# Kernel optimization log

Measured on AMD Instinct MI355X. Metric: run time of the kernel, lower is better.

The kernel has to match this reference:

```python
import jax, jax.numpy as jnp
import numpy as np

H = 1024   # hidden_size
L = 2      # num_layers
T = 32     # num_tracks
B = 512    # batch


def setup_inputs() -> dict:
    key = jax.random.key(0)
    ks = jax.random.split(key, 8)
    s = 1.0 / np.sqrt(H)  # PyTorch LSTM/Linear init scale
    z = jax.random.normal(ks[0], (B, H), jnp.float32)
    W_ih = jax.random.uniform(ks[1], (L, 4 * H, H), jnp.float32, -s, s)
    W_hh = jax.random.uniform(ks[2], (L, 4 * H, H), jnp.float32, -s, s)
    b_ih = jax.random.uniform(ks[3], (L, 4 * H), jnp.float32, -s, s)
    b_hh = jax.random.uniform(ks[4], (L, 4 * H), jnp.float32, -s, s)
    to_h_W = jax.random.uniform(ks[5], (L * H, H), jnp.float32, -s, s)
    to_h_b = jax.random.uniform(ks[6], (L * H,), jnp.float32, -s, s)
    init_emb = jax.random.normal(ks[7], (1, H), jnp.float32)  # nn.Embedding(1, H)
    return {"z": z, "to_h_W": to_h_W, "to_h_b": to_h_b, "init_emb": init_emb,
            "W_ih": W_ih, "W_hh": W_hh, "b_ih": b_ih, "b_hh": b_hh}


def reference(z, to_h_W, to_h_b, init_emb, W_ih, W_hh, b_ih, b_hh):
    bsz = z.shape[0]
    # h init from z: [B, L*H] -> [L, B, H]; c init zeros
    h0 = jnp.tanh(z @ to_h_W.T + to_h_b).reshape(bsz, L, H).transpose(1, 0, 2)
    c0 = jnp.zeros_like(h0)
    # initial input token embedding (index 0 for all batch entries)
    x0 = jnp.broadcast_to(init_emb[0], (bsz, H))

    def step(carry, _):
        x, h, c = carry
        hs, cs = [], []
        for l in range(L):  # fixed small layer loop
            # PyTorch gate order: i, f, g, o
            gates = x @ W_ih[l].T + b_ih[l] + h[l] @ W_hh[l].T + b_hh[l]
            i_g, f_g, g_g, o_g = jnp.split(gates, 4, axis=-1)
            c_new = jax.nn.sigmoid(f_g) * c[l] + jax.nn.sigmoid(i_g) * jnp.tanh(g_g)
            h_new = jax.nn.sigmoid(o_g) * jnp.tanh(c_new)
            hs.append(h_new)
            cs.append(c_new)
            x = h_new  # output of layer l is input of layer l+1
        return (x, jnp.stack(hs), jnp.stack(cs)), x

    _, ys = jax.lax.scan(step, (x0, h0, c0), None, length=T)
    return ys  # [T, B, H] == stacked list of per-track embeddings
```

## Files before the change

### kernel.cpp

```cpp
#include <hip/hip_runtime.h>
#include <cstdint>

typedef __attribute__((ext_vector_type(8))) short short8;
typedef __attribute__((ext_vector_type(4))) float f32x4;
typedef unsigned short u16;

#define HD 1024
#define BSZ 512
#define NL 2
#define TSTEPS 32
#define BM 64
#define BN 128
#define BK 64

__device__ __forceinline__ u16 f2bf(float x) {
  union { float f; uint32_t u; } v; v.f = x;
  uint32_t r = v.u + 0x7FFFu + ((v.u >> 16) & 1u);
  return (u16)(r >> 16);
}
__device__ __forceinline__ float sigm(float x) { return 1.f / (1.f + __expf(-x)); }
__device__ __forceinline__ float tanhfast(float x) { return 1.f - 2.f / (__expf(2.f * x) + 1.f); }

__global__ void pack_w2(const float* __restrict__ Wih, const float* __restrict__ Whh,
                        u16* __restrict__ W2) {
  int idx = blockIdx.x * 256 + threadIdx.x;
  int l   = idx >> 20;
  int rem = idx & 0xFFFFF;
  int np  = rem >> 8;
  int k   = (rem & 255) << 3;
  int gate = (np >> 4) & 3;
  int j    = ((np >> 6) << 4) | (np & 15);
  int n    = (gate << 10) | j;
  const float* src = (k < HD) ? (Wih + ((size_t)(l * 4096 + n) << 10) + k)
                              : (Whh + ((size_t)(l * 4096 + n) << 10) + (k - HD));
  float4 a = reinterpret_cast<const float4*>(src)[0];
  float4 b = reinterpret_cast<const float4*>(src)[1];
  union { u16 s[8]; short8 v; } o;
  o.s[0]=f2bf(a.x); o.s[1]=f2bf(a.y); o.s[2]=f2bf(a.z); o.s[3]=f2bf(a.w);
  o.s[4]=f2bf(b.x); o.s[5]=f2bf(b.y); o.s[6]=f2bf(b.z); o.s[7]=f2bf(b.w);
  *reinterpret_cast<short8*>(W2 + (((size_t)l * 4096 + np) << 11) + k) = o.v;
}

__global__ void pack_thw(const float* __restrict__ thw, u16* __restrict__ dst) {
  int idx = blockIdx.x * 256 + threadIdx.x;
  size_t off = (size_t)idx << 3;
  float4 a = reinterpret_cast<const float4*>(thw + off)[0];
  float4 b = reinterpret_cast<const float4*>(thw + off)[1];
  union { u16 s[8]; short8 v; } o;
  o.s[0]=f2bf(a.x); o.s[1]=f2bf(a.y); o.s[2]=f2bf(a.z); o.s[3]=f2bf(a.w);
  o.s[4]=f2bf(b.x); o.s[5]=f2bf(b.y); o.s[6]=f2bf(b.z); o.s[7]=f2bf(b.w);
  *reinterpret_cast<short8*>(dst + off) = o.v;
}

__global__ void pack_small(const float* __restrict__ z, const float* __restrict__ emb,
                           const float* __restrict__ bih, const float* __restrict__ bhh,
                           u16* __restrict__ zb, u16* __restrict__ xb,
                           float* __restrict__ bias2) {
  int idx = blockIdx.x * 256 + threadIdx.x;
  if (idx < 65536) {
    size_t off = (size_t)idx << 3;
    float4 a = reinterpret_cast<const float4*>(z + off)[0];
    float4 b = reinterpret_cast<const float4*>(z + off)[1];
    union { u16 s[8]; short8 v; } o;
    o.s[0]=f2bf(a.x); o.s[1]=f2bf(a.y); o.s[2]=f2bf(a.z); o.s[3]=f2bf(a.w);
    o.s[4]=f2bf(b.x); o.s[5]=f2bf(b.y); o.s[6]=f2bf(b.z); o.s[7]=f2bf(b.w);
    *reinterpret_cast<short8*>(zb + off) = o.v;
  } else if (idx < 131072) {
    size_t off = (size_t)(idx - 65536) << 3;
    int k = (int)(off & 1023);
    float4 a = reinterpret_cast<const float4*>(emb + k)[0];
    float4 b = reinterpret_cast<const float4*>(emb + k)[1];
    union { u16 s[8]; short8 v; } o;
    o.s[0]=f2bf(a.x); o.s[1]=f2bf(a.y); o.s[2]=f2bf(a.z); o.s[3]=f2bf(a.w);
    o.s[4]=f2bf(b.x); o.s[5]=f2bf(b.y); o.s[6]=f2bf(b.z); o.s[7]=f2bf(b.w);
    *reinterpret_cast<short8*>(xb + off) = o.v;
  } else if (idx < 139264) {
    int q = idx - 131072;
    int l = q >> 12, np = q & 4095;
    int gate = (np >> 4) & 3;
    int j    = ((np >> 6) << 4) | (np & 15);
    int n    = (gate << 10) | j;
    bias2[(l << 12) + np] = bih[(l << 12) + n] + bhh[(l << 12) + n];
  }
}

template<int EPI>
__global__ __launch_bounds__(256, 1)
void lstm_gemm(const u16* __restrict__ A0, const u16* __restrict__ A1,
               const u16* __restrict__ W, const float* __restrict__ bias,
               float* __restrict__ cb0, float* __restrict__ cb1,
               u16* __restrict__ hb0, u16* __restrict__ hb1,
               float* __restrict__ yout, int K)
{
  __shared__ u16 smem[3 * 12288];
  const int tid  = threadIdx.x;
  const int lane = tid & 63;
  const int wave = tid >> 6;
  const int wr = wave >> 1, wc = wave & 1;
  const int lr = lane & 15, lk = lane >> 4;

  int bx, by;
  if constexpr (EPI == 0) {
    bx = blockIdx.x & 15; by = blockIdx.x >> 4;
  } else {
    int xcd = blockIdx.x & 7, win = blockIdx.x >> 3;
    bx = xcd * 4 + (win >> 3);
    by = win & 7;
  }
  const int m0 = by * BM;
  const int n0 = bx * BN;

  f32x4 acc[2][4];
  #pragma unroll
  for (int a = 0; a < 2; ++a)
    #pragma unroll
    for (int b = 0; b < 4; ++b) acc[a][b] = (f32x4){0.f, 0.f, 0.f, 0.f};

  auto stage = [&](int buf, int kt) {
    const int k0 = kt * BK;
    u16* Ad = smem + buf * 12288;
    u16* Bd = Ad + 4096;
    const u16* Aptr; int kk;
    if (k0 < 1024) { Aptr = A0; kk = k0; } else { Aptr = A1; kk = k0 - 1024; }
    #pragma unroll
    for (int i = 0; i < 2; ++i) {
      int d = i * 256 + tid;
      int r = d >> 3, cd = d & 7;
      int cs = cd ^ (r & 7);
      const u16* g = Aptr + (((size_t)(m0 + r)) << 10) + kk + cs * 8;
      __builtin_amdgcn_global_load_lds((const __attribute__((address_space(1))) void*)g,
                                       (__attribute__((address_space(3))) void*)(Ad + d * 8),
                                       16, 0, 0);
    }
    #pragma unroll
    for (int i = 0; i < 4; ++i) {
      int d = i * 256 + tid;
      int r = d >> 3, cd = d & 7;
      int cs = cd ^ (r & 7);
      const u16* g = W + (size_t)(n0 + r) * K + k0 + cs * 8;
      __builtin_amdgcn_global_load_lds((const __attribute__((address_space(1))) void*)g,
                                       (__attribute__((address_space(3))) void*)(Bd + d * 8),
                                       16, 0, 0);
    }
  };

  const int NT = K / BK;
  stage(0, 0);
  stage(1, 1);

  for (int kt = 0; kt < NT; ++kt) {
    if (kt + 2 < NT) {
      stage((kt + 2) % 3, kt + 2);
      asm volatile("s_waitcnt vmcnt(12)" ::: "memory");
    } else if (kt + 1 < NT) {
      asm volatile("s_waitcnt vmcnt(6)" ::: "memory");
    } else {
      asm volatile("s_waitcnt vmcnt(0)" ::: "memory");
    }
    __builtin_amdgcn_s_barrier();
    __builtin_amdgcn_sched_barrier(0);

    const u16* Asb = smem + (kt % 3) * 12288;
    const u16* Bsb = Asb + 4096;
    #pragma unroll
    for (int ks = 0; ks < 2; ++ks) {
      const int sw = (ks * 4 + lk) ^ (lr & 7);
      short8 a[2], b[4];
      #pragma unroll
      for (int mi = 0; mi < 2; ++mi) {
        const int ra = wr * 32 + mi * 16 + lr;
        a[mi] = *reinterpret_cast<const short8*>(Asb + ra * 64 + sw * 8);
      }
      #pragma unroll
      for (int g = 0; g < 4; ++g) {
        const int rb = wc * 64 + g * 16 + lr;
        b[g] = *reinterpret_cast<const short8*>(Bsb + rb * 64 + sw * 8);
      }
      #pragma unroll
      for (int mi = 0; mi < 2; ++mi)
        #pragma unroll
        for (int g = 0; g < 4; ++g)
          acc[mi][g] = __builtin_amdgcn_mfma_f32_16x16x32_bf16(a[mi], b[g], acc[mi][g], 0, 0, 0);
    }
    asm volatile("s_waitcnt lgkmcnt(0)" ::: "memory");
    __builtin_amdgcn_s_barrier();
    __builtin_amdgcn_sched_barrier(0);
  }

  if constexpr (EPI == 0) {
    #pragma unroll
    for (int g = 0; g < 4; ++g) {
      int n = n0 + wc * 64 + g * 16 + lr;
      float bn = bias[n];
      int lsel = n >> 10, j = n & 1023;
      float* cb = lsel ? cb1 : cb0;
      u16*   hb = lsel ? hb1 : hb0;
      #pragma unroll
      for (int mi = 0; mi < 2; ++mi)
        #pragma unroll
        for (int i = 0; i < 4; ++i) {
          int r = m0 + wr * 32 + mi * 16 + lk * 4 + i;
          size_t idx = ((size_t)r << 10) + j;
          hb[idx] = f2bf(tanhfast(acc[mi][g][i] + bn));
          cb[idx] = 0.f;
        }
    }
  } else {
    float bi = bias[n0 + wc * 64 +  0 + lr];
    float bf = bias[n0 + wc * 64 + 16 + lr];
    float bg = bias[n0 + wc * 64 + 32 + lr];
    float bo = bias[n0 + wc * 64 + 48 + lr];
    int j = (bx * 2 + wc) * 16 + lr;
    #pragma unroll
    for (int mi = 0; mi < 2; ++mi)
      #pragma unroll
      for (int i = 0; i < 4; ++i) {
        int r = m0 + wr * 32 + mi * 16 + lk * 4 + i;
        size_t idx = ((size_t)r << 10) + j;
        float ig = sigm(acc[mi][0][i] + bi);
        float fg = sigm(acc[mi][1][i] + bf);
        float gg = tanhfast(acc[mi][2][i] + bg);
        float og = sigm(acc[mi][3][i] + bo);
        float cn = fg * cb0[idx] + ig * gg;
        cb0[idx] = cn;
        float hn = og * tanhfast(cn);
        hb0[idx] = f2bf(hn);
        if constexpr (EPI == 2) yout[idx] = hn;
      }
  }
}

extern "C" void kernel_launch(void* const* d_in, const int* in_sizes, int n_in,
                              void* d_out, int out_size, void* d_ws, size_t ws_size,
                              hipStream_t stream) {
  const float* z   = (const float*)d_in[0];
  const float* thw = (const float*)d_in[1];
  const float* thb = (const float*)d_in[2];
  const float* emb = (const float*)d_in[3];
  const float* Wih = (const float*)d_in[4];
  const float* Whh = (const float*)d_in[5];
  const float* bih = (const float*)d_in[6];
  const float* bhh = (const float*)d_in[7];
  float* out = (float*)d_out;

  char* ws = (char*)d_ws;
  size_t off = 0;
  auto carve = [&](size_t bytes) { char* p = ws + off; off += (bytes + 255) & ~(size_t)255; return p; };
  u16* W2     = (u16*)carve((size_t)NL * 4096 * 2048 * 2);
  u16* thwb   = (u16*)carve((size_t)2048 * 1024 * 2);
  u16* zb     = (u16*)carve((size_t)BSZ * HD * 2);
  u16* xb     = (u16*)carve((size_t)BSZ * HD * 2);
  u16* h0b0   = (u16*)carve((size_t)BSZ * HD * 2);
  u16* h0b1   = (u16*)carve((size_t)BSZ * HD * 2);
  u16* h1b0   = (u16*)carve((size_t)BSZ * HD * 2);
  u16* h1b1   = (u16*)carve((size_t)BSZ * HD * 2);
  float* c0   = (float*)carve((size_t)BSZ * HD * 4);
  float* c1   = (float*)carve((size_t)BSZ * HD * 4);
  float* bias2 = (float*)carve((size_t)NL * 4096 * 4);
  if (off > ws_size) return;

  u16* h0b[2] = { h0b0, h0b1 };
  u16* h1b[2] = { h1b0, h1b1 };

  pack_w2   <<<8192, 256, 0, stream>>>(Wih, Whh, W2);
  pack_thw  <<<1024, 256, 0, stream>>>(thw, thwb);
  pack_small<<< 544, 256, 0, stream>>>(z, emb, bih, bhh, zb, xb, bias2);

  lstm_gemm<0><<<128, 256, 0, stream>>>(zb, zb, thwb, thb,
                                        c0, c1, h0b[0], h1b[0], nullptr, 1024);

  for (int t = 0; t < TSTEPS; ++t) {
    const u16* xs = (t == 0) ? xb : h1b[t & 1];
    lstm_gemm<1><<<256, 256, 0, stream>>>(
        xs, h0b[t & 1], W2, bias2,
        c0, nullptr, h0b[(t + 1) & 1], nullptr, nullptr, 2048);
    lstm_gemm<2><<<256, 256, 0, stream>>>(
        h0b[(t + 1) & 1], h1b[t & 1], W2 + (size_t)4096 * 2048, bias2 + 4096,
        c1, nullptr, h1b[(t + 1) & 1], nullptr, out + (size_t)t * BSZ * HD, 2048);
  }
}
```

Before: 1.341 ms.

## Fuse all LSTM timesteps into a persistent kernel with flag-based synchronization

Replaces the per-timestep, per-layer kernel launches with one persistent kernel in which each block loops over all timesteps and both layers, synchronizing on per-row-block atomic counters instead of kernel boundaries. Cell state is kept in registers rather than read from and written to global memory each step. The initial GEMM is split into its own kernel. This removes launch overhead and c-state memory traffic, but relies on all 256 blocks being co-resident and adds spin-wait and fence costs.

```diff
diff --git a/kernel.cpp b/kernel.cpp
--- a/kernel.cpp
+++ b/kernel.cpp
@@ -55,7 +55,7 @@
 __global__ void pack_small(const float* __restrict__ z, const float* __restrict__ emb,
                            const float* __restrict__ bih, const float* __restrict__ bhh,
                            u16* __restrict__ zb, u16* __restrict__ xb,
-                           float* __restrict__ bias2) {
+                           float* __restrict__ bias2, int* __restrict__ flags) {
   int idx = blockIdx.x * 256 + threadIdx.x;
   if (idx < 65536) {
     size_t off = (size_t)idx << 3;
@@ -81,36 +81,32 @@
     int j    = ((np >> 6) << 4) | (np & 15);
     int n    = (gate << 10) | j;
     bias2[(l << 12) + np] = bih[(l << 12) + n] + bhh[(l << 12) + n];
-  }
-}
-
-template<int EPI>
-__global__ __launch_bounds__(256, 1)
-void lstm_gemm(const u16* __restrict__ A0, const u16* __restrict__ A1,
-               const u16* __restrict__ W, const float* __restrict__ bias,
-               float* __restrict__ cb0, float* __restrict__ cb1,
-               u16* __restrict__ hb0, u16* __restrict__ hb1,
-               float* __restrict__ yout, int K)
+  } else if (idx < 139776) {
+    flags[idx - 139264] = 0;
+  }
+}
+
+__device__ __forceinline__ void post_flag(int* f, int tid) {
+  __threadfence();
+  __syncthreads();
+  if (tid == 0) __hip_atomic_fetch_add(f, 1, __ATOMIC_RELEASE, __HIP_MEMORY_SCOPE_AGENT);
+}
+__device__ __forceinline__ void wait_flag(int* f, int target, int tid) {
+  if (tid == 0) {
+    while (__hip_atomic_load(f, __ATOMIC_ACQUIRE, __HIP_MEMORY_SCOPE_AGENT) < target)
+      __builtin_amdgcn_s_sleep(2);
+  }
+  __syncthreads();
+  __builtin_amdgcn_sched_barrier(0);
+}
+
+template<int K>
+__device__ __forceinline__ void gemm_tile(
+    u16* __restrict__ smem, const u16* __restrict__ A0, const u16* __restrict__ A1,
+    const u16* __restrict__ Wb, int m0, int tid, int wr, int wc, int lr, int lk,
+    f32x4 (&acc)[2][4])
 {
-  __shared__ u16 smem[3 * 12288];
-  const int tid  = threadIdx.x;
-  const int lane = tid & 63;
-  const int wave = tid >> 6;
-  const int wr = wave >> 1, wc = wave & 1;
-  const int lr = lane & 15, lk = lane >> 4;
-
-  int bx, by;
-  if constexpr (EPI == 0) {
-    bx = blockIdx.x & 15; by = blockIdx.x >> 4;
-  } else {
-    int xcd = blockIdx.x & 7, win = blockIdx.x >> 3;
-    bx = xcd * 4 + (win >> 3);
-    by = win & 7;
-  }
-  const int m0 = by * BM;
-  const int n0 = bx * BN;
-
-  f32x4 acc[2][4];
+  constexpr int NT = K / BK;
   #pragma unroll
   for (int a = 0; a < 2; ++a)
     #pragma unroll
@@ -137,14 +133,13 @@
       int d = i * 256 + tid;
       int r = d >> 3, cd = d & 7;
       int cs = cd ^ (r & 7);
-      const u16* g = W + (size_t)(n0 + r) * K + k0 + cs * 8;
+      const u16* g = Wb + (size_t)r * K + k0 + cs * 8;
       __builtin_amdgcn_global_load_lds((const __attribute__((address_space(1))) void*)g,
                                        (__attribute__((address_space(3))) void*)(Bd + d * 8),
                                        16, 0, 0);
     }
   };
 
-  const int NT = K / BK;
   stage(0, 0);
   stage(1, 1);
 
@@ -167,15 +162,11 @@
       const int sw = (ks * 4 + lk) ^ (lr & 7);
       short8 a[2], b[4];
       #pragma unroll
-      for (int mi = 0; mi < 2; ++mi) {
-        const int ra = wr * 32 + mi * 16 + lr;
-        a[mi] = *reinterpret_cast<const short8*>(Asb + ra * 64 + sw * 8);
-      }
-      #pragma unroll
-      for (int g = 0; g < 4; ++g) {
-        const int rb = wc * 64 + g * 16 + lr;
-        b[g] = *reinterpret_cast<const short8*>(Bsb + rb * 64 + sw * 8);
-      }
+      for (int mi = 0; mi < 2; ++mi)
+        a[mi] = *reinterpret_cast<const short8*>(Asb + (wr * 32 + mi * 16 + lr) * 64 + sw * 8);
+      #pragma unroll
+      for (int g = 0; g < 4; ++g)
+        b[g] = *reinterpret_cast<const short8*>(Bsb + (wc * 64 + g * 16 + lr) * 64 + sw * 8);
       #pragma unroll
       for (int mi = 0; mi < 2; ++mi)
         #pragma unroll
@@ -186,47 +177,116 @@
     __builtin_amdgcn_s_barrier();
     __builtin_amdgcn_sched_barrier(0);
   }
-
-  if constexpr (EPI == 0) {
-    #pragma unroll
-    for (int g = 0; g < 4; ++g) {
-      int n = n0 + wc * 64 + g * 16 + lr;
-      float bn = bias[n];
-      int lsel = n >> 10, j = n & 1023;
-      float* cb = lsel ? cb1 : cb0;
-      u16*   hb = lsel ? hb1 : hb0;
-      #pragma unroll
-      for (int mi = 0; mi < 2; ++mi)
-        #pragma unroll
-        for (int i = 0; i < 4; ++i) {
-          int r = m0 + wr * 32 + mi * 16 + lk * 4 + i;
-          size_t idx = ((size_t)r << 10) + j;
-          hb[idx] = f2bf(tanhfast(acc[mi][g][i] + bn));
-          cb[idx] = 0.f;
-        }
-    }
-  } else {
-    float bi = bias[n0 + wc * 64 +  0 + lr];
-    float bf = bias[n0 + wc * 64 + 16 + lr];
-    float bg = bias[n0 + wc * 64 + 32 + lr];
-    float bo = bias[n0 + wc * 64 + 48 + lr];
-    int j = (bx * 2 + wc) * 16 + lr;
+}
+
+__global__ __launch_bounds__(256, 1)
+void init_gemm(const u16* __restrict__ zb, const u16* __restrict__ thwb,
+               const float* __restrict__ thb, u16* __restrict__ h0, u16* __restrict__ h1) {
+  __shared__ u16 smem[3 * 12288];
+  const int tid  = threadIdx.x;
+  const int lane = tid & 63, wave = tid >> 6;
+  const int wr = wave >> 1, wc = wave & 1;
+  const int lr = lane & 15, lk = lane >> 4;
+  const int bx = blockIdx.x & 15, by = blockIdx.x >> 4;
+  const int m0 = by * BM, n0 = bx * BN;
+
+  f32x4 acc[2][4];
+  gemm_tile<1024>(smem, zb, zb, thwb + (size_t)n0 * 1024, m0, tid, wr, wc, lr, lk, acc);
+
+  #pragma unroll
+  for (int g = 0; g < 4; ++g) {
+    int n = n0 + wc * 64 + g * 16 + lr;
+    float bn = thb[n];
+    int lsel = n >> 10, j = n & 1023;
+    u16* hb = lsel ? h1 : h0;
     #pragma unroll
     for (int mi = 0; mi < 2; ++mi)
       #pragma unroll
       for (int i = 0; i < 4; ++i) {
         int r = m0 + wr * 32 + mi * 16 + lk * 4 + i;
-        size_t idx = ((size_t)r << 10) + j;
-        float ig = sigm(acc[mi][0][i] + bi);
-        float fg = sigm(acc[mi][1][i] + bf);
-        float gg = tanhfast(acc[mi][2][i] + bg);
-        float og = sigm(acc[mi][3][i] + bo);
-        float cn = fg * cb0[idx] + ig * gg;
-        cb0[idx] = cn;
+        hb[((size_t)r << 10) + j] = f2bf(tanhfast(acc[mi][g][i] + bn));
+      }
+  }
+}
+
+__global__ __launch_bounds__(256, 1)
+void lstm_persistent(const u16* __restrict__ xb,
+                     const u16* __restrict__ W2, const float* __restrict__ bias2,
+                     u16* __restrict__ h0a, u16* __restrict__ h0c,
+                     u16* __restrict__ h1a, u16* __restrict__ h1c,
+                     float* __restrict__ yout, int* __restrict__ f0, int* __restrict__ f1)
+{
+  __shared__ u16 smem[3 * 12288];
+  const int tid  = threadIdx.x;
+  const int lane = tid & 63, wave = tid >> 6;
+  const int wr = wave >> 1, wc = wave & 1;
+  const int lr = lane & 15, lk = lane >> 4;
+  const int xcd = blockIdx.x & 7, win = blockIdx.x >> 3;
+  const int bx = xcd * 4 + (win >> 3);
+  const int by = win & 7;
+  const int m0 = by * BM, n0 = bx * BN;
+
+  const u16* Wl0 = W2 + (size_t)n0 * 2048;
+  const u16* Wl1 = W2 + (size_t)4096 * 2048 + (size_t)n0 * 2048;
+  const float b0i = bias2[n0 + wc * 64 +  0 + lr];
+  const float b0f = bias2[n0 + wc * 64 + 16 + lr];
+  const float b0g = bias2[n0 + wc * 64 + 32 + lr];
+  const float b0o = bias2[n0 + wc * 64 + 48 + lr];
+  const float b1i = bias2[4096 + n0 + wc * 64 +  0 + lr];
+  const float b1f = bias2[4096 + n0 + wc * 64 + 16 + lr];
+  const float b1g = bias2[4096 + n0 + wc * 64 + 32 + lr];
+  const float b1o = bias2[4096 + n0 + wc * 64 + 48 + lr];
+  const int j = (bx * 2 + wc) * 16 + lr;
+
+  float c0r[2][4] = {{0.f,0.f,0.f,0.f},{0.f,0.f,0.f,0.f}};
+  float c1r[2][4] = {{0.f,0.f,0.f,0.f},{0.f,0.f,0.f,0.f}};
+  f32x4 acc[2][4];
+
+  for (int t = 0; t < TSTEPS; ++t) {
+    const int p = t & 1;
+    const u16* h0_rd = p ? h0c : h0a;
+    u16*       h0_wr = p ? h0a : h0c;
+    const u16* h1_rd = p ? h1c : h1a;
+    u16*       h1_wr = p ? h1a : h1c;
+    const u16* x     = (t == 0) ? xb : h1_rd;
+
+    if (t > 0) wait_flag(&f1[(t - 1) * 8 + by], 32, tid);
+
+    gemm_tile<2048>(smem, x, h0_rd, Wl0, m0, tid, wr, wc, lr, lk, acc);
+    #pragma unroll
+    for (int mi = 0; mi < 2; ++mi)
+      #pragma unroll
+      for (int i = 0; i < 4; ++i) {
+        int r = m0 + wr * 32 + mi * 16 + lk * 4 + i;
+        float ig = sigm(acc[mi][0][i] + b0i);
+        float fg = sigm(acc[mi][1][i] + b0f);
+        float gg = tanhfast(acc[mi][2][i] + b0g);
+        float og = sigm(acc[mi][3][i] + b0o);
+        float cn = fg * c0r[mi][i] + ig * gg;
+        c0r[mi][i] = cn;
+        h0_wr[((size_t)r << 10) + j] = f2bf(og * tanhfast(cn));
+      }
+    post_flag(&f0[t * 8 + by], tid);
+    wait_flag(&f0[t * 8 + by], 32, tid);
+
+    gemm_tile<2048>(smem, h0_wr, h1_rd, Wl1, m0, tid, wr, wc, lr, lk, acc);
+    float* yt = yout + ((size_t)t << 19);
+    #pragma unroll
+    for (int mi = 0; mi < 2; ++mi)
+      #pragma unroll
+      for (int i = 0; i < 4; ++i) {
+        int r = m0 + wr * 32 + mi * 16 + lk * 4 + i;
+        float ig = sigm(acc[mi][0][i] + b1i);
+        float fg = sigm(acc[mi][1][i] + b1f);
+        float gg = tanhfast(acc[mi][2][i] + b1g);
+        float og = sigm(acc[mi][3][i] + b1o);
+        float cn = fg * c1r[mi][i] + ig * gg;
+        c1r[mi][i] = cn;
         float hn = og * tanhfast(cn);
-        hb0[idx] = f2bf(hn);
-        if constexpr (EPI == 2) yout[idx] = hn;
+        h1_wr[((size_t)r << 10) + j] = f2bf(hn);
+        yt[((size_t)r << 10) + j] = hn;
       }
+    post_flag(&f1[t * 8 + by], tid);
   }
 }
 
@@ -246,36 +306,26 @@
   char* ws = (char*)d_ws;
   size_t off = 0;
   auto carve = [&](size_t bytes) { char* p = ws + off; off += (bytes + 255) & ~(size_t)255; return p; };
-  u16* W2     = (u16*)carve((size_t)NL * 4096 * 2048 * 2);
-  u16* thwb   = (u16*)carve((size_t)2048 * 1024 * 2);
-  u16* zb     = (u16*)carve((size_t)BSZ * HD * 2);
-  u16* xb     = (u16*)carve((size_t)BSZ * HD * 2);
-  u16* h0b0   = (u16*)carve((size_t)BSZ * HD * 2);
-  u16* h0b1   = (u16*)carve((size_t)BSZ * HD * 2);
-  u16* h1b0   = (u16*)carve((size_t)BSZ * HD * 2);
-  u16* h1b1   = (u16*)carve((size_t)BSZ * HD * 2);
-  float* c0   = (float*)carve((size_t)BSZ * HD * 4);
-  float* c1   = (float*)carve((size_t)BSZ * HD * 4);
+  u16* W2      = (u16*)carve((size_t)NL * 4096 * 2048 * 2);
+  u16* thwb    = (u16*)carve((size_t)2048 * 1024 * 2);
+  u16* zb      = (u16*)carve((size_t)BSZ * HD * 2);
+  u16* xb      = (u16*)carve((size_t)BSZ * HD * 2);
+  u16* h0a     = (u16*)carve((size_t)BSZ * HD * 2);
+  u16* h0c     = (u16*)carve((size_t)BSZ * HD * 2);
+  u16* h1a     = (u16*)carve((size_t)BSZ * HD * 2);
+  u16* h1c     = (u16*)carve((size_t)BSZ * HD * 2);
   float* bias2 = (float*)carve((size_t)NL * 4096 * 4);
+  int* flags   = (int*)carve(2 * TSTEPS * 8 * 4);
   if (off > ws_size) return;
-
-  u16* h0b[2] = { h0b0, h0b1 };
-  u16* h1b[2] = { h1b0, h1b1 };
+  int* f0 = flags;
+  int* f1 = flags + TSTEPS * 8;
 
   pack_w2   <<<8192, 256, 0, stream>>>(Wih, Whh, W2);
   pack_thw  <<<1024, 256, 0, stream>>>(thw, thwb);
-  pack_small<<< 544, 256, 0, stream>>>(z, emb, bih, bhh, zb, xb, bias2);
-
-  lstm_gemm<0><<<128, 256, 0, stream>>>(zb, zb, thwb, thb,
-                                        c0, c1, h0b[0], h1b[0], nullptr, 1024);
-
-  for (int t = 0; t < TSTEPS; ++t) {
-    const u16* xs = (t == 0) ? xb : h1b[t & 1];
-    lstm_gemm<1><<<256, 256, 0, stream>>>(
-        xs, h0b[t & 1], W2, bias2,
-        c0, nullptr, h0b[(t + 1) & 1], nullptr, nullptr, 2048);
-    lstm_gemm<2><<<256, 256, 0, stream>>>(
-        h0b[(t + 1) & 1], h1b[t & 1], W2 + (size_t)4096 * 2048, bias2 + 4096,
-        c1, nullptr, h1b[(t + 1) & 1], nullptr, out + (size_t)t * BSZ * HD, 2048);
-  }
-}
+  pack_small<<< 546, 256, 0, stream>>>(z, emb, bih, bhh, zb, xb, bias2, flags);
+
+  init_gemm<<<128, 256, 0, stream>>>(zb, thwb, thb, h0a, h1a);
+
+  lstm_persistent<<<256, 256, 0, stream>>>(xb, W2, bias2, h0a, h0c, h1a, h1c,
+                                           out, f0, f1);
+}
```

After: 3.862 ms. 188% more time.
